# Kernel tuning notes

Hardware: AMD Instinct MI355X
Metric: run time of the kernel (lower is better)

Reference implementation:

```python
import jax, jax.numpy as jnp
import numpy as np

BASE = 10000.0

def _rope(x):
    # x: [b, n, h, d]; positions along token axis n, rotate-half convention
    d = x.shape[-1]
    n = x.shape[1]
    inv_freq = 1.0 / (BASE ** (jnp.arange(0, d, 2, dtype=jnp.float32) / d))  # [d/2]
    t = jnp.arange(n, dtype=jnp.float32)
    freqs = jnp.outer(t, inv_freq)                       # [n, d/2]
    emb = jnp.concatenate([freqs, freqs], axis=-1)       # [n, d]
    cos = jnp.cos(emb)[None, :, None, :]
    sin = jnp.sin(emb)[None, :, None, :]
    x1, x2 = jnp.split(x, 2, axis=-1)
    rot = jnp.concatenate([-x2, x1], axis=-1)
    return x * cos + rot * sin


def setup_inputs() -> dict:
    key = jax.random.key(0)
    k1, k2, k3 = jax.random.split(key, 3)
    b, c, hh, ww = 64, 1024, 16, 16
    x = jax.random.normal(k1, (b, c, hh, ww), dtype=jnp.float32)
    w_qkv = jax.random.normal(k2, (3 * c, c), dtype=jnp.float32) * 0.02
    w_lin = jax.random.normal(k3, (c, c, 1, 1), dtype=jnp.float32) * 0.02
    b_lin = jnp.zeros((c,), dtype=jnp.float32)
    return {"x": x, "w_qkv": w_qkv, "w_lin": w_lin, "b_lin": b_lin, "n_heads": 16}


def reference(x, w_qkv, w_lin, b_lin, n_heads):
    b, c, hh, ww = x.shape
    n = hh * ww
    d_head = c // n_heads
    scale = d_head ** -0.5
    # flatten(2).transpose(-2,-1): [b, n, c]
    xt = jnp.transpose(x.reshape(b, c, n), (0, 2, 1))
    # qkv proj, unflatten to [b, n, heads, 3*d_head], chunk along last dim
    qkv = (xt @ w_qkv.T).reshape(b, n, n_heads, 3 * d_head)
    q, k, v = jnp.split(qkv, 3, axis=-1)                  # each [b, n, h, d]
    q = _rope(q)
    k = _rope(k)
    q = jax.nn.softmax(q, axis=-1) * scale                # softmax over d_head
    k = jax.nn.softmax(k, axis=-2)                        # softmax over heads axis (as in torch code)
    # k^T @ v over the heads axis -> per-token [d_head, d_head] context
    context = jnp.einsum('bnhd,bnhe->bnde', k, v)
    o = jnp.einsum('bnhd,bnde->bnhe', q, context)         # [b, n, h, d]
    # transpose(-2,-1).reshape(b, c, h, w)
    o = jnp.transpose(o, (0, 1, 3, 2)).reshape(b, c, hh, ww)
    # 1x1 conv
    return jnp.einsum('bchw,oc->bohw', o, w_lin[:, :, 0, 0]) + b_lin[None, :, None, None]
```

## Files before the change

kernel.cpp:

```cpp
#include <hip/hip_runtime.h>
#include <hip/hip_bf16.h>
#include <math.h>

typedef __hip_bfloat16 hbf16;
typedef __attribute__((ext_vector_type(8))) __bf16    bf16x8;
typedef __attribute__((ext_vector_type(4))) float     f32x4;
typedef __attribute__((ext_vector_type(4))) _Float16  f16x4;
typedef __attribute__((ext_vector_type(8))) unsigned short u16x8;

#define C_    1024
#define NTOK  256
#define NH    16
#define J3    3072

__device__ __forceinline__ unsigned short fbits(float v){
    return __builtin_bit_cast(unsigned short, __float2bfloat16(v));
}
__device__ __forceinline__ __bf16 to_bf(float v){
    return __builtin_bit_cast(__bf16, __float2bfloat16(v));
}

__device__ __forceinline__ void gload_lds16(const __bf16* g, __bf16* l) {
    __builtin_amdgcn_global_load_lds((const __attribute__((address_space(1))) void*)g,
                                     (__attribute__((address_space(3))) void*)l, 16, 0, 0);
}

__global__ __launch_bounds__(256) void cvt_w(const float* __restrict__ wq,
                                             __bf16* __restrict__ wqo,
                                             const float* __restrict__ wl,
                                             __bf16* __restrict__ wlo) {
    const float* in; __bf16* out; int i;
    if (blockIdx.x < 3072) { in = wq; out = wqo; i = blockIdx.x * 256 + threadIdx.x; }
    else                   { in = wl; out = wlo; i = (blockIdx.x - 3072) * 256 + threadIdx.x; }
    float4 v = ((const float4*)in)[i];
    ushort4 u;
    u.x = fbits(v.x); u.y = fbits(v.y); u.z = fbits(v.z); u.w = fbits(v.w);
    ((ushort4*)out)[i] = u;
}

__global__ __launch_bounds__(256) void xpose_x(const float* __restrict__ X,
                                               __bf16* __restrict__ Xt) {
    __shared__ float t[32][36];
    const int b = blockIdx.z, k0 = blockIdx.y * 32, s0 = blockIdx.x * 32;
    const int tid = threadIdx.x;
    {
        int kl = tid >> 3, s4 = (tid & 7) * 4;
        float4 v = *(const float4*)(X + ((size_t)b << 18) + (size_t)(k0 + kl) * 256 + s0 + s4);
        t[kl][s4] = v.x; t[kl][s4 + 1] = v.y; t[kl][s4 + 2] = v.z; t[kl][s4 + 3] = v.w;
    }
    __syncthreads();
    {
        int sl = tid >> 3, k4 = (tid & 7) * 4;
        ushort4 u;
        u.x = fbits(t[k4][sl]); u.y = fbits(t[k4 + 1][sl]);
        u.z = fbits(t[k4 + 2][sl]); u.w = fbits(t[k4 + 3][sl]);
        *(ushort4*)(Xt + (size_t)(b * 256 + s0 + sl) * 1024 + k0 + k4) = u;
    }
}

#define WAITVM_I(N) asm volatile("s_waitcnt vmcnt(" #N ")" ::: "memory")
#define WAITVM(N) WAITVM_I(N)

__device__ __forceinline__ void stage_unit(const __bf16* __restrict__ G,
                                           __bf16* l, int kk, int wave, int lane) {
    const int rl = lane >> 2;
    const int cg = (lane & 3) ^ ((lane >> 3) & 3);
    const int coff = kk + cg * 8;
    #pragma unroll
    for (int i = 0; i < 2; ++i) {
        const int seg = wave * 2 + i;
        const int row = seg * 16 + rl;
        gload_lds16(G + ((size_t)row << 10) + coff, l + seg * 512);
    }
}

#define BARRIER()                                                              \
    __builtin_amdgcn_sched_barrier(0);                                         \
    __builtin_amdgcn_s_barrier();                                              \
    __builtin_amdgcn_sched_barrier(0)

#define STEP(BUF, S, DOSTG, VM)                                                \
  {                                                                            \
    const __bf16* sa_ = sm.kl + (BUF) * 16384 + aoff;                          \
    const __bf16* sb_ = sm.kl + (BUF) * 16384 + 8192 + boff;                   \
    bf16x8 bfr[4], afr[4];                                                     \
                               \
    _Pragma("unroll") for (int ni = 0; ni < 4; ++ni)                           \
        bfr[ni] = *(const bf16x8*)(sb_ + ni * 512);                            \
    _Pragma("unroll") for (int mi = 0; mi < 4; ++mi)                           \
        afr[mi] = *(const bf16x8*)(sa_ + mi * 512);                            \
    if (DOSTG) stage_unit(Ab, sm.kl + (((S) + 3) & 3) * 16384,                 \
                          ((S) + 3) << 5, wave, lane);                         \
    BARRIER();                                                                 \
    __builtin_amdgcn_s_setprio(1);                                             \
    _Pragma("unroll") for (int mi = 0; mi < 4; ++mi)                           \
      _Pragma("unroll") for (int ni = 0; ni < 4; ++ni)                         \
        acc[mi][ni] = __builtin_amdgcn_mfma_f32_16x16x32_bf16(                 \
            afr[mi], bfr[ni], acc[mi][ni], 0, 0, 0);                           \
    __builtin_amdgcn_s_setprio(0);                                             \
    BARRIER();                                                                 \
                                      \
    _Pragma("unroll") for (int mi = 0; mi < 4; ++mi)                           \
        afr[mi] = *(const bf16x8*)(sa_ + (mi + 4) * 512);                      \
    if (DOSTG) stage_unit(Bb, sm.kl + (((S) + 3) & 3) * 16384 + 8192,          \
                          ((S) + 3) << 5, wave, lane);                         \
    BARRIER();                                                                 \
    __builtin_amdgcn_s_setprio(1);                                             \
    _Pragma("unroll") for (int mi = 0; mi < 4; ++mi)                           \
      _Pragma("unroll") for (int ni = 0; ni < 4; ++ni)                         \
        acc[mi + 4][ni] = __builtin_amdgcn_mfma_f32_16x16x32_bf16(             \
            afr[mi], bfr[ni], acc[mi + 4][ni], 0, 0, 0);                       \
    __builtin_amdgcn_s_setprio(0);                                             \
    WAITVM(VM);                                                                \
    BARRIER();                                                                 \
  }

template <int EPI>
__global__ __launch_bounds__(512, 2) void gemm256(const __bf16* __restrict__ A,
                                                  const __bf16* __restrict__ B,
                                                  void* __restrict__ Cout,
                                                  const float* __restrict__ bias) {
    __shared__ union __align__(16) {
        __bf16 kl[4 * 16384];
        __bf16 st[128][264];
    } sm;

    const int tid  = threadIdx.x;
    const int wave = tid >> 6, lane = tid & 63;
    const int wm = wave >> 2, wn = wave & 3;
    const int quad = lane >> 4, m = lane & 15;

    const int wg = blockIdx.x;
    int mb, nb;
    if (EPI == 0) {
        const int local = wg >> 3;
        mb = (wg & 7) * 8 + (local & 7);
        nb = local >> 3;
    } else {
        const int local = wg >> 3;
        mb = local & 3;
        nb = (wg & 7) * 8 + (local >> 2);
    }
    const int m0 = mb << 8, n0 = nb << 8;

    const __bf16* Ab = A + ((size_t)m0 << 10);
    const __bf16* Bb = B + ((size_t)n0 << 10);

    const int pcs  = quad ^ ((lane >> 1) & 3);
    const int aoff = (wm * 128 + m) * 32 + pcs * 8;
    const int boff = (wn * 64  + m) * 32 + pcs * 8;

    f32x4 acc[8][4] = {};

    stage_unit(Ab, sm.kl,                 0,  wave, lane);
    stage_unit(Bb, sm.kl + 8192,          0,  wave, lane);
    stage_unit(Ab, sm.kl + 16384,         32, wave, lane);
    stage_unit(Bb, sm.kl + 16384 + 8192,  32, wave, lane);
    stage_unit(Ab, sm.kl + 32768,         64, wave, lane);
    stage_unit(Bb, sm.kl + 32768 + 8192,  64, wave, lane);
    WAITVM(8);
    BARRIER();

    for (int tt = 0; tt < 28; tt += 4) {
        STEP(0, tt + 0, 1, 8)
        STEP(1, tt + 1, 1, 8)
        STEP(2, tt + 2, 1, 8)
        STEP(3, tt + 3, 1, 8)
    }
    STEP(0, 28, 1, 8)
    STEP(1, 29, 0, 4)
    STEP(2, 30, 0, 0)
    STEP(3, 31, 0, 0)

    if (EPI == 0) {
        __syncthreads();
        __bf16* Y = (__bf16*)Cout;
        #pragma unroll
        for (int h = 0; h < 2; ++h) {
            if (wm == h) {
                #pragma unroll
                for (int mi = 0; mi < 8; ++mi)
                    #pragma unroll
                    for (int ni = 0; ni < 4; ++ni) {
                        const int r = mi * 16 + quad * 4;
                        const int c = wn * 64 + ni * 16 + m;
                        #pragma unroll
                        for (int j = 0; j < 4; ++j)
                            sm.st[r + j][c] = to_bf(acc[mi][ni][j]);
                    }
            }
            __syncthreads();
            #pragma unroll
            for (int i = 0; i < 8; ++i) {
                const int cid = i * 512 + tid;
                const int r = cid >> 5, ch = (cid & 31) * 8;
                *(bf16x8*)(Y + (size_t)(m0 + h * 128 + r) * 3072 + n0 + ch) =
                    *(const bf16x8*)&sm.st[r][ch];
            }
            __syncthreads();
        }
    } else {
        float* outp = (float*)Cout;
        const int cl = lane & 15, rq = lane >> 4;
        const int rbase = m0 + wm * 128 + rq * 4;
        const int nbase = n0 + wn * 64 + cl;
        #pragma unroll
        for (int mi = 0; mi < 8; ++mi) {
            float bia[4];
            #pragma unroll
            for (int j = 0; j < 4; ++j) bia[j] = bias[rbase + mi * 16 + j];
            #pragma unroll
            for (int ni = 0; ni < 4; ++ni) {
                const int nn = nbase + ni * 16;
                const size_t base = ((size_t)(nn >> 8) << 18) + (nn & 255);
                #pragma unroll
                for (int j = 0; j < 4; ++j) {
                    const int oc = rbase + mi * 16 + j;
                    outp[base + ((size_t)oc << 8)] = acc[mi][ni][j] + bia[j];
                }
            }
        }
    }
}

__global__ __launch_bounds__(1024) void attn_mfma(const __bf16* __restrict__ Y,
                                                  __bf16* __restrict__ Ot) {
    __shared__ union __align__(16) {
        __bf16  v[16][1024];
        ushort4 ost[256][16];
    } sm;

    const int tid  = threadIdx.x;
    const int wave = tid >> 6, lane = tid & 63;
    const int bb = blockIdx.x >> 4;
    const int n0 = (blockIdx.x & 15) * 16;
    const int n  = n0 + wave;
    const int quad = lane >> 4, m = lane & 15;
    const __bf16* Yt = Y + (size_t)(bb * 256 + n) * J3;

    #pragma unroll
    for (int p = 0; p < 2; ++p) {
        const int h = p * 8 + (lane >> 3), part = lane & 7;
        gload_lds16(Yt + h * 192 + 128 + part * 8, &sm.v[wave][p * 512]);
    }

    bf16x8 qb[2], kb[2];
    #pragma unroll
    for (int st = 0; st < 2; ++st) {
        qb[st] = *(const bf16x8*)(Yt + m * 192 +      st * 32 + quad * 8);
        kb[st] = *(const bf16x8*)(Yt + m * 192 + 64 + st * 32 + quad * 8);
    }
    float qf[16], kf[16];
    #pragma unroll
    for (int st = 0; st < 2; ++st)
        #pragma unroll
        for (int j = 0; j < 8; ++j) {
            qf[st * 8 + j] = (float)qb[st][j];
            kf[st * 8 + j] = (float)kb[st][j];
        }

    const float fn = (float)n;
    #pragma unroll
    for (int j = 0; j < 8; ++j) {
        const float d  = (float)(quad * 8 + j);
        const float th = fn * __expf(-0.28782313662425572f * d);
        const float sn = __sinf(th), cn = __cosf(th);
        float a0 = qf[j], a1 = qf[8 + j];
        qf[j]     = a0 * cn - a1 * sn;
        qf[8 + j] = a1 * cn + a0 * sn;
        float b0 = kf[j], b1 = kf[8 + j];
        kf[j]     = b0 * cn - b1 * sn;
        kf[8 + j] = b1 * cn + b0 * sn;
    }

    float qe[16], ls = 0.f;
    #pragma unroll
    for (int i = 0; i < 16; ++i) { qe[i] = __expf(qf[i]); ls += qe[i]; }
    ls += __shfl_xor(ls, 16);
    ls += __shfl_xor(ls, 32);
    const float qinv = 0.125f * __builtin_amdgcn_rcpf(ls);
    bf16x8 qbh[2];
    #pragma unroll
    for (int st = 0; st < 2; ++st)
        #pragma unroll
        for (int j = 0; j < 8; ++j) qbh[st][j] = to_bf(qe[st * 8 + j] * qinv);

    float ke[16], kc[16];
    #pragma unroll
    for (int i = 0; i < 16; ++i) { ke[i] = __expf(kf[i]); kc[i] = ke[i]; }
    #pragma unroll
    for (int msk = 1; msk <= 8; msk <<= 1)
        #pragma unroll
        for (int i = 0; i < 16; ++i) kc[i] += __shfl_xor(kc[i], msk);
    bf16x8 kbh[2];
    #pragma unroll
    for (int st = 0; st < 2; ++st)
        #pragma unroll
        for (int j = 0; j < 8; ++j)
            kbh[st][j] = to_bf(ke[st * 8 + j] * __builtin_amdgcn_rcpf(kc[st * 8 + j]));

    f32x4 Sp = {0.f, 0.f, 0.f, 0.f};
    Sp = __builtin_amdgcn_mfma_f32_16x16x32_bf16(kbh[0], qbh[0], Sp, 0, 0, 0);
    Sp = __builtin_amdgcn_mfma_f32_16x16x32_bf16(kbh[1], qbh[1], Sp, 0, 0, 0);

    __syncthreads();

    f32x4 o4[4];
#if __has_builtin(__builtin_amdgcn_mfma_f32_16x16x16f16)
    f16x4 af;
    #pragma unroll
    for (int r = 0; r < 4; ++r) af[r] = (_Float16)Sp[r];
    #pragma unroll
    for (int tile = 0; tile < 4; ++tile) {
        f16x4 bv;
        #pragma unroll
        for (int j = 0; j < 4; ++j)
            bv[j] = (_Float16)(float)sm.v[wave][(quad * 4 + j) * 64 + tile * 16 + m];
        f32x4 z = {0.f, 0.f, 0.f, 0.f};
        o4[tile] = __builtin_amdgcn_mfma_f32_16x16x16f16(af, bv, z, 0, 0, 0);
    }
#else
    bf16x8 a2;
    #pragma unroll
    for (int j = 0; j < 8; ++j) {
        int k = quad * 8 + j;
        int src = ((k & 15) >> 2) * 16 + m;
        float v = __shfl(Sp[k & 3], src, 64);
        a2[j] = (quad < 2) ? to_bf(v) : to_bf(0.f);
    }
    #pragma unroll
    for (int tile = 0; tile < 4; ++tile) {
        bf16x8 bv;
        #pragma unroll
        for (int j = 0; j < 8; ++j) {
            int k = quad * 8 + j;
            int kk = (k < 16) ? k : 0;
            bv[j] = sm.v[wave][kk * 64 + tile * 16 + m];
        }
        f32x4 z = {0.f, 0.f, 0.f, 0.f};
        o4[tile] = __builtin_amdgcn_mfma_f32_16x16x32_bf16(a2, bv, z, 0, 0, 0);
    }
#endif

    __syncthreads();

    #pragma unroll
    for (int r = 0; r < 4; ++r) {
        const int s = m * 16 + quad * 4 + r;
        const int phys = wave ^ (quad * 4 + r) ^ m;
        ushort4 u;
        u.x = fbits(o4[0][r]); u.y = fbits(o4[1][r]);
        u.z = fbits(o4[2][r]); u.w = fbits(o4[3][r]);
        sm.ost[s][phys] = u;
    }
    __syncthreads();

    {
        const int row = tid >> 2;
        const int w0  = (tid & 3) * 4;
        ushort4 u4[4];
        #pragma unroll
        for (int j = 0; j < 4; ++j) {
            const int phys = (w0 + j) ^ (row & 15) ^ (row >> 4);
            u4[j] = sm.ost[row][phys];
        }
        __bf16* dst = Ot + (((size_t)(bb * 256 + row)) << 10) + n0 * 4 + w0 * 4;
        u16x8 a = {u4[0].x, u4[0].y, u4[0].z, u4[0].w, u4[1].x, u4[1].y, u4[1].z, u4[1].w};
        u16x8 b = {u4[2].x, u4[2].y, u4[2].z, u4[2].w, u4[3].x, u4[3].y, u4[3].z, u4[3].w};
        *(u16x8*)dst = a;
        *(u16x8*)(dst + 8) = b;
    }
}

extern "C" void kernel_launch(void* const* d_in, const int* in_sizes, int n_in,
                              void* d_out, int out_size, void* d_ws, size_t ws_size,
                              hipStream_t stream) {
    const float* x     = (const float*)d_in[0];
    const float* w_qkv = (const float*)d_in[1];
    const float* w_lin = (const float*)d_in[2];
    const float* b_lin = (const float*)d_in[3];
    float* out = (float*)d_out;

    char* ws = (char*)d_ws;
    __bf16* Y    = (__bf16*)ws;
    __bf16* XtOt = (__bf16*)(ws + (size_t)100663296);
    __bf16* Wqb  = (__bf16*)(ws + (size_t)134217728);
    __bf16* Wlb  = (__bf16*)(ws + (size_t)140509184);

    cvt_w<<<4096, 256, 0, stream>>>(w_qkv, Wqb, w_lin, Wlb);
    xpose_x<<<dim3(8, 32, 64), 256, 0, stream>>>(x, XtOt);

    gemm256<0><<<768, 512, 0, stream>>>(XtOt, Wqb, (void*)Y, nullptr);
    attn_mfma<<<1024, 1024, 0, stream>>>(Y, XtOt);
    gemm256<1><<<256, 512, 0, stream>>>(Wlb, XtOt, (void*)out, b_lin);
}
```

Baseline: 313.1 us.

## Restructure 256x256 GEMM to 16 waves with double-buffered LDS pipeline

Both GEMMs now run with 1024 threads (16 waves) per block instead of 8. Each wave owns a 64x64 sub-tile, so accumulator registers drop from 8x4 to 4x4 fragments. The 4-stage LDS ring with split A/B staging becomes a 2-buffer scheme: one wait and barrier per k-step, and the next tile is issued right after compute. This aims to hide latency with more waves, but gives only a shallow prefetch depth and the new launch bounds may limit residency.

```diff
diff --git a/kernel.cpp b/kernel.cpp
--- a/kernel.cpp
+++ b/kernel.cpp
@@ -61,37 +61,30 @@
 #define WAITVM_I(N) asm volatile("s_waitcnt vmcnt(" #N ")" ::: "memory")
 #define WAITVM(N) WAITVM_I(N)
 
-__device__ __forceinline__ void stage_unit(const __bf16* __restrict__ G,
-                                           __bf16* l, int kk, int wave, int lane) {
-    const int rl = lane >> 2;
-    const int cg = (lane & 3) ^ ((lane >> 3) & 3);
-    const int coff = kk + cg * 8;
-    #pragma unroll
-    for (int i = 0; i < 2; ++i) {
-        const int seg = wave * 2 + i;
-        const int row = seg * 16 + rl;
-        gload_lds16(G + ((size_t)row << 10) + coff, l + seg * 512);
-    }
-}
-
 #define BARRIER()                                                              \
     __builtin_amdgcn_sched_barrier(0);                                         \
     __builtin_amdgcn_s_barrier();                                              \
     __builtin_amdgcn_sched_barrier(0)
 
+__device__ __forceinline__ void stage16(const __bf16* __restrict__ G,
+                                        __bf16* l, int kk, int wave, int lane) {
+    const int rl = lane >> 2;
+    const int cg = (lane & 3) ^ ((lane >> 3) & 3);
+    const int row = wave * 16 + rl;
+    gload_lds16(G + ((size_t)row << 10) + kk + cg * 8, l + wave * 512);
+}
+
 #define STEP(BUF, S, DOSTG, VM)                                                \
   {                                                                            \
-    const __bf16* sa_ = sm.kl + (BUF) * 16384 + aoff;                          \
-    const __bf16* sb_ = sm.kl + (BUF) * 16384 + 8192 + boff;                   \
-    bf16x8 bfr[4], afr[4];                                                     \
-                               \
-    _Pragma("unroll") for (int ni = 0; ni < 4; ++ni)                           \
-        bfr[ni] = *(const bf16x8*)(sb_ + ni * 512);                            \
-    _Pragma("unroll") for (int mi = 0; mi < 4; ++mi)                           \
-        afr[mi] = *(const bf16x8*)(sa_ + mi * 512);                            \
-    if (DOSTG) stage_unit(Ab, sm.kl + (((S) + 3) & 3) * 16384,                 \
-                          ((S) + 3) << 5, wave, lane);                         \
+    WAITVM(VM);                                                                \
     BARRIER();                                                                 \
+    const __bf16* sa_ = sm.kl[BUF] + aoff;                                     \
+    const __bf16* sb_ = sm.kl[BUF] + 8192 + boff;                              \
+    bf16x8 afr[4], bfr[4];                                                     \
+    _Pragma("unroll") for (int i = 0; i < 4; ++i) {                            \
+      afr[i] = *(const bf16x8*)(sa_ + i * 512);                                \
+      bfr[i] = *(const bf16x8*)(sb_ + i * 512);                                \
+    }                                                                          \
     __builtin_amdgcn_s_setprio(1);                                             \
     _Pragma("unroll") for (int mi = 0; mi < 4; ++mi)                           \
       _Pragma("unroll") for (int ni = 0; ni < 4; ++ni)                         \
@@ -99,29 +92,19 @@
             afr[mi], bfr[ni], acc[mi][ni], 0, 0, 0);                           \
     __builtin_amdgcn_s_setprio(0);                                             \
     BARRIER();                                                                 \
-                                      \
-    _Pragma("unroll") for (int mi = 0; mi < 4; ++mi)                           \
-        afr[mi] = *(const bf16x8*)(sa_ + (mi + 4) * 512);                      \
-    if (DOSTG) stage_unit(Bb, sm.kl + (((S) + 3) & 3) * 16384 + 8192,          \
-                          ((S) + 3) << 5, wave, lane);                         \
-    BARRIER();                                                                 \
-    __builtin_amdgcn_s_setprio(1);                                             \
-    _Pragma("unroll") for (int mi = 0; mi < 4; ++mi)                           \
-      _Pragma("unroll") for (int ni = 0; ni < 4; ++ni)                         \
-        acc[mi + 4][ni] = __builtin_amdgcn_mfma_f32_16x16x32_bf16(             \
-            afr[mi], bfr[ni], acc[mi + 4][ni], 0, 0, 0);                       \
-    __builtin_amdgcn_s_setprio(0);                                             \
-    WAITVM(VM);                                                                \
-    BARRIER();                                                                 \
+    if (DOSTG) {                                                               \
+      stage16(Ab, &sm.kl[BUF][0],    ((S) + 2) << 5, wave, lane);              \
+      stage16(Bb, &sm.kl[BUF][8192], ((S) + 2) << 5, wave, lane);              \
+    }                                                                          \
   }
 
 template <int EPI>
-__global__ __launch_bounds__(512, 2) void gemm256(const __bf16* __restrict__ A,
-                                                  const __bf16* __restrict__ B,
-                                                  void* __restrict__ Cout,
-                                                  const float* __restrict__ bias) {
+__global__ __launch_bounds__(1024, 4) void gemm256(const __bf16* __restrict__ A,
+                                                   const __bf16* __restrict__ B,
+                                                   void* __restrict__ Cout,
+                                                   const float* __restrict__ bias) {
     __shared__ union __align__(16) {
-        __bf16 kl[4 * 16384];
+        __bf16 kl[2][16384];
         __bf16 st[128][264];
     } sm;
 
@@ -146,43 +129,37 @@
     const __bf16* Ab = A + ((size_t)m0 << 10);
     const __bf16* Bb = B + ((size_t)n0 << 10);
 
-    const int pcs  = quad ^ ((lane >> 1) & 3);
-    const int aoff = (wm * 128 + m) * 32 + pcs * 8;
-    const int boff = (wn * 64  + m) * 32 + pcs * 8;
-
-    f32x4 acc[8][4] = {};
-
-    stage_unit(Ab, sm.kl,                 0,  wave, lane);
-    stage_unit(Bb, sm.kl + 8192,          0,  wave, lane);
-    stage_unit(Ab, sm.kl + 16384,         32, wave, lane);
-    stage_unit(Bb, sm.kl + 16384 + 8192,  32, wave, lane);
-    stage_unit(Ab, sm.kl + 32768,         64, wave, lane);
-    stage_unit(Bb, sm.kl + 32768 + 8192,  64, wave, lane);
-    WAITVM(8);
-    BARRIER();
-
-    for (int tt = 0; tt < 28; tt += 4) {
-        STEP(0, tt + 0, 1, 8)
-        STEP(1, tt + 1, 1, 8)
-        STEP(2, tt + 2, 1, 8)
-        STEP(3, tt + 3, 1, 8)
-    }
-    STEP(0, 28, 1, 8)
-    STEP(1, 29, 0, 4)
-    STEP(2, 30, 0, 0)
-    STEP(3, 31, 0, 0)
+    const int pcs  = quad ^ ((m >> 1) & 3);
+    const int aoff = (wm * 64 + m) * 32 + pcs * 8;
+    const int boff = (wn * 64 + m) * 32 + pcs * 8;
+
+    f32x4 acc[4][4] = {};
+
+    stage16(Ab, &sm.kl[0][0],    0,  wave, lane);
+    stage16(Bb, &sm.kl[0][8192], 0,  wave, lane);
+    stage16(Ab, &sm.kl[1][0],    32, wave, lane);
+    stage16(Bb, &sm.kl[1][8192], 32, wave, lane);
+
+    for (int tt = 0; tt < 28; tt += 2) {
+        STEP(0, tt + 0, 1, 2)
+        STEP(1, tt + 1, 1, 2)
+    }
+    STEP(0, 28, 1, 2)
+    STEP(1, 29, 1, 2)
+    STEP(0, 30, 0, 2)
+    STEP(1, 31, 0, 0)
 
     if (EPI == 0) {
         __syncthreads();
         __bf16* Y = (__bf16*)Cout;
         #pragma unroll
         for (int h = 0; h < 2; ++h) {
-            if (wm == h) {
+            if ((wm >> 1) == h) {
                 #pragma unroll
-                for (int mi = 0; mi < 8; ++mi)
+                for (int mi = 0; mi < 4; ++mi)
                     #pragma unroll
                     for (int ni = 0; ni < 4; ++ni) {
-                        const int r = mi * 16 + quad * 4;
+                        const int r = (wm & 1) * 64 + mi * 16 + quad * 4;
                         const int c = wn * 64 + ni * 16 + m;
                         #pragma unroll
                         for (int j = 0; j < 4; ++j)
@@ -191,8 +168,8 @@
             }
             __syncthreads();
             #pragma unroll
-            for (int i = 0; i < 8; ++i) {
-                const int cid = i * 512 + tid;
+            for (int i = 0; i < 4; ++i) {
+                const int cid = i * 1024 + tid;
                 const int r = cid >> 5, ch = (cid & 31) * 8;
                 *(bf16x8*)(Y + (size_t)(m0 + h * 128 + r) * 3072 + n0 + ch) =
                     *(const bf16x8*)&sm.st[r][ch];
@@ -201,11 +178,10 @@
         }
     } else {
         float* outp = (float*)Cout;
-        const int cl = lane & 15, rq = lane >> 4;
-        const int rbase = m0 + wm * 128 + rq * 4;
-        const int nbase = n0 + wn * 64 + cl;
-        #pragma unroll
-        for (int mi = 0; mi < 8; ++mi) {
+        const int rbase = m0 + wm * 64 + quad * 4;
+        const int nbase = n0 + wn * 64 + m;
+        #pragma unroll
+        for (int mi = 0; mi < 4; ++mi) {
             float bia[4];
             #pragma unroll
             for (int j = 0; j < 4; ++j) bia[j] = bias[rbase + mi * 16 + j];
@@ -390,7 +366,7 @@
     cvt_w<<<4096, 256, 0, stream>>>(w_qkv, Wqb, w_lin, Wlb);
     xpose_x<<<dim3(8, 32, 64), 256, 0, stream>>>(x, XtOt);
 
-    gemm256<0><<<768, 512, 0, stream>>>(XtOt, Wqb, (void*)Y, nullptr);
+    gemm256<0><<<768, 1024, 0, stream>>>(XtOt, Wqb, (void*)Y, nullptr);
     attn_mfma<<<1024, 1024, 0, stream>>>(Y, XtOt);
-    gemm256<1><<<256, 512, 0, stream>>>(Wlb, XtOt, (void*)out, b_lin);
-}
+    gemm256<1><<<256, 1024, 0, stream>>>(Wlb, XtOt, (void*)out, b_lin);
+}
```

Result: no change. 313.2 us (+0.0%).
